# Kernel tuning notes

Hardware: AMD Instinct MI355X
Metric: run time of the kernel (lower is better)

The kernel has to match this reference:

```python
import jax, jax.numpy as jnp
import numpy as np

N = 50000      # nodes
E = 800000     # edges (avg degree 16)
D = 128        # hidden dim (hidden_dim = [128,128,128])
G = 500        # graphs in batch
NS = 100       # num_stock
M0 = 64        # mid_dim[0] == mid_dim[1]
M2 = 1         # mid_dim[2]
LRELU_SLOPE = 0.2
BN_EPS = 1e-5


def setup_inputs() -> dict:
    key = jax.random.key(0)
    ks = jax.random.split(key, 24)
    s = 0.05
    inp = {
        "x": jax.random.normal(ks[0], (N, D), dtype=jnp.float32),
        "graph_data": jax.random.randint(ks[1], (2, E), 0, N, dtype=jnp.int64)
            if jax.config.read("jax_enable_x64") else jax.random.randint(ks[1], (2, E), 0, N).astype(jnp.int32),
        "batch": jnp.sort(jax.random.randint(ks[2], (N,), 0, G)).astype(jnp.int32),
        # GATv2Conv layer 0 (in=D, out=D, heads=1)
        "wl0": jax.random.normal(ks[3], (D, D)) * s,
        "bl0": jax.random.normal(ks[4], (D,)) * s,
        "wr0": jax.random.normal(ks[5], (D, D)) * s,
        "br0": jax.random.normal(ks[6], (D,)) * s,
        "att0": jax.random.normal(ks[7], (D,)) * s,
        "b0": jax.random.normal(ks[8], (D,)) * s,
        # GATv2Conv layer 1
        "wl1": jax.random.normal(ks[9], (D, D)) * s,
        "bl1": jax.random.normal(ks[10], (D,)) * s,
        "wr1": jax.random.normal(ks[11], (D, D)) * s,
        "br1": jax.random.normal(ks[12], (D,)) * s,
        "att1": jax.random.normal(ks[13], (D,)) * s,
        "b1": jax.random.normal(ks[14], (D,)) * s,
        # BatchNorm1d (eval mode, running stats) applied after layer 0 only
        "bn_gamma": jnp.ones((D,), jnp.float32),
        "bn_beta": jnp.zeros((D,), jnp.float32),
        "bn_mean": jax.random.normal(ks[15], (D,)) * 0.1,
        "bn_var": jax.random.uniform(ks[16], (D,), minval=0.5, maxval=1.5),
        # fc1: hidden_dim[-2] -> num_stock*mid_dim[0]; fc3: mid_dim[1] -> mid_dim[2]
        "fc1_w": jax.random.normal(ks[17], (D, NS * M0)) * s,
        "fc1_b": jax.random.normal(ks[18], (NS * M0,)) * s,
        "fc3_w": jax.random.normal(ks[19], (M0, M2)) * s,
        "fc3_b": jax.random.normal(ks[20], (M2,)) * s,
    }
    return inp


def _gatv2(x, src, dst, wl, bl, wr, br, att, b):
    """PyG GATv2Conv, heads=1, add_self_loops=False, eval mode (no dropout)."""
    xl = x @ wl + bl                      # source-side transform [N, D]
    xr = x @ wr + br                      # target-side transform [N, D]
    # per-edge attention logits: a^T LeakyReLU(x_j + x_i)
    e = jnp.einsum("ed,d->e", jax.nn.leaky_relu(xl[src] + xr[dst], LRELU_SLOPE), att)
    # softmax over incoming edges of each destination node
    m = jax.ops.segment_max(e, dst, num_segments=N)
    m = jnp.where(jnp.isfinite(m), m, 0.0)
    p = jnp.exp(e - m[dst])
    denom = jax.ops.segment_sum(p, dst, num_segments=N)
    alpha = p / denom[dst]
    out = jax.ops.segment_sum(alpha[:, None] * xl[src], dst, num_segments=N)
    return out + b


def reference(x, graph_data, batch, wl0, bl0, wr0, br0, att0, b0,
              wl1, bl1, wr1, br1, att1, b1,
              bn_gamma, bn_beta, bn_mean, bn_var,
              fc1_w, fc1_b, fc3_w, fc3_b):
    src, dst = graph_data[0], graph_data[1]
    # layer 0: GATv2 -> BatchNorm (eval) -> ReLU
    h = _gatv2(x, src, dst, wl0, bl0, wr0, br0, att0, b0)
    h = bn_gamma * (h - bn_mean) * jax.lax.rsqrt(bn_var + BN_EPS) + bn_beta
    h = jax.nn.relu(h)
    # layer 1 (last): GATv2 only
    h = _gatv2(h, src, dst, wl1, bl1, wr1, br1, att1, b1)
    # global mean pool over graphs
    counts = jax.ops.segment_sum(jnp.ones((N,), h.dtype), batch, num_segments=G)
    pooled = jax.ops.segment_sum(h, batch, num_segments=G) / jnp.maximum(counts, 1.0)[:, None]
    # fc1 + reshape to [G, num_stock, mid_dim0]; dropout is eval-mode identity
    h = jax.nn.relu(pooled @ fc1_w + fc1_b).reshape(G, NS, M0)
    out = jax.nn.sigmoid(h @ fc3_w + fc3_b)   # [G, NS, 1]
    return out.reshape(G, NS * M2)
```

## Files before the change

### kernel.cpp

```cpp
#include <hip/hip_runtime.h>

#define DD 128
#define GG 500
#define NSTK 100
#define SLOPE 0.2f
#define BN_EPS 1e-5f
#define XPAD 136
#define SLOT 64

typedef __attribute__((ext_vector_type(8))) short bf16x8;
typedef __attribute__((ext_vector_type(4))) float f32x4;
typedef __attribute__((ext_vector_type(2))) float f32x2;
typedef unsigned int uint;
typedef unsigned short ushort;

static __device__ __forceinline__ ushort f2bf(float f) {
    union { float f; unsigned int u; } v; v.f = f;
    unsigned int r = (v.u + 0x7fff + ((v.u >> 16) & 1)) >> 16;
    return (ushort)r;
}

static __device__ __forceinline__ f32x2 bfpair(uint u) {
    union { uint2 u2; f32x2 f; } c;
    c.u2.x = u << 16;
    c.u2.y = u & 0xffff0000u;
    return c.f;
}


__global__ __launch_bounds__(128) void wprep_kernel(
    const float* __restrict__ wl0, const float* __restrict__ wr0,
    const float* __restrict__ wl1, const float* __restrict__ wr1,
    ushort* __restrict__ wt0, ushort* __restrict__ wt1,
    const float* __restrict__ bn_g, const float* __restrict__ bn_b,
    const float* __restrict__ bn_m, const float* __restrict__ bn_v,
    float* __restrict__ bn_scale, float* __restrict__ bn_shift)
{
    int c = blockIdx.x;
    int layer = blockIdx.y;
    int k = threadIdx.x;
    const float* wl = layer ? wl1 : wl0;
    const float* wr = layer ? wr1 : wr0;
    float v = (c < 128) ? wl[k * DD + c] : wr[k * DD + (c - 128)];
    (layer ? wt1 : wt0)[c * DD + k] = f2bf(v);
    if (c == 0 && layer == 0) {
        float s = bn_g[k] * rsqrtf(bn_v[k] + BN_EPS);
        bn_scale[k] = s;
        bn_shift[k] = bn_b[k] - bn_m[k] * s;
    }
}


__global__ __launch_bounds__(256) void mm0_scat_kernel(
    const int* __restrict__ src, const int* __restrict__ dst,
    int* __restrict__ deg, ushort* __restrict__ csr, int e_count, int MB,
    const float* __restrict__ x, const ushort* __restrict__ wt,
    const float* __restrict__ bA, const float* __restrict__ bB,
    ushort* __restrict__ outA, ushort* __restrict__ outB, int n)
{
    if ((int)blockIdx.x >= MB) {
        int e = ((int)blockIdx.x - MB) * 256 + threadIdx.x;
        if (e < e_count) {
            int d = dst[e];
            int r = atomicAdd(&deg[d], 1);
            if (r < SLOT) csr[d * SLOT + r] = (ushort)src[e];
        }
        return;
    }
    __shared__ ushort xs[32 * XPAD];
    int t = threadIdx.x;
    int row0 = (int)blockIdx.x * 32;

    #pragma unroll
    for (int i = 0; i < 2; ++i) {
        int idx8 = i * 256 + t;
        int r = idx8 >> 4;
        int c = (idx8 & 15) * 8;
        float4 v0 = make_float4(0.f, 0.f, 0.f, 0.f), v1 = v0;
        if (row0 + r < n) {
            v0 = *(const float4*)&x[(size_t)(row0 + r) * DD + c];
            v1 = *(const float4*)&x[(size_t)(row0 + r) * DD + c + 4];
        }
        union { bf16x8 v; ushort u[8]; } pk;
        pk.u[0] = f2bf(v0.x); pk.u[1] = f2bf(v0.y); pk.u[2] = f2bf(v0.z); pk.u[3] = f2bf(v0.w);
        pk.u[4] = f2bf(v1.x); pk.u[5] = f2bf(v1.y); pk.u[6] = f2bf(v1.z); pk.u[7] = f2bf(v1.w);
        *(bf16x8*)&xs[r * XPAD + c] = pk.v;
    }
    __syncthreads();

    int wave = t >> 6, lane = t & 63;
    int m16 = lane & 15;
    int kg = lane >> 4;

    bf16x8 bfr[4][4];
    #pragma unroll
    for (int ct = 0; ct < 4; ++ct) {
        int c = wave * 64 + ct * 16 + m16;
        #pragma unroll
        for (int ks = 0; ks < 4; ++ks)
            bfr[ks][ct] = *(const bf16x8*)&wt[(size_t)c * DD + ks * 32 + kg * 8];
    }

    f32x4 acc[2][4];
    #pragma unroll
    for (int rt = 0; rt < 2; ++rt)
        #pragma unroll
        for (int ct = 0; ct < 4; ++ct) acc[rt][ct] = (f32x4){0.f, 0.f, 0.f, 0.f};

    #pragma unroll
    for (int ks = 0; ks < 4; ++ks) {
        int koff = ks * 32 + kg * 8;
        bf16x8 a[2];
        #pragma unroll
        for (int rt = 0; rt < 2; ++rt)
            a[rt] = *(bf16x8*)&xs[(rt * 16 + m16) * XPAD + koff];
        #pragma unroll
        for (int rt = 0; rt < 2; ++rt)
            #pragma unroll
            for (int ct = 0; ct < 4; ++ct)
                acc[rt][ct] = __builtin_amdgcn_mfma_f32_16x16x32_bf16(a[rt], bfr[ks][ct], acc[rt][ct], 0, 0, 0);
    }

    #pragma unroll
    for (int rt = 0; rt < 2; ++rt) {
        int r0 = row0 + rt * 16 + kg * 4;
        #pragma unroll
        for (int ct = 0; ct < 4; ++ct) {
            int c = wave * 64 + ct * 16 + m16;
            float bb; ushort* op; int cc;
            if (c < 128) { bb = bA[c]; op = outA; cc = c; }
            else         { bb = bB[c - 128]; op = outB; cc = c - 128; }
            #pragma unroll
            for (int i = 0; i < 4; ++i) {
                if (r0 + i < n)
                    op[(size_t)(r0 + i) * DD + cc] = f2bf(acc[rt][ct][i] + bb);
            }
        }
    }
}


__global__ __launch_bounds__(256) void gat_agg_kernel(
    const ushort* __restrict__ xl, const ushort* __restrict__ xr,
    const int* __restrict__ degv, const ushort* __restrict__ csr,
    const float* __restrict__ att, const float* __restrict__ bias,
    const float* __restrict__ bn_scale, const float* __restrict__ bn_shift,
    ushort* __restrict__ out_bf, float* __restrict__ out_f32,
    int n, int use_bn)
{
    int wave = (int)((blockIdx.x * 256 + threadIdx.x) >> 6);
    int lane = threadIdx.x & 63;
    if (wave >= n) return;
    int grp = lane >> 4;
    int gl  = lane & 15;
    int f   = gl * 8;

    int deg = degv[wave];
    if (deg > SLOT) deg = SLOT;
    int sv = (lane < deg) ? (int)csr[(size_t)wave * SLOT + lane] : 0;

    uint4 xru = *(const uint4*)&xr[(size_t)wave * DD + f];
    f32x2 xrp[4] = {bfpair(xru.x), bfpair(xru.y), bfpair(xru.z), bfpair(xru.w)};
    const f32x2* attp = (const f32x2*)&att[f];
    f32x2 atp[4] = {attp[0], attp[1], attp[2], attp[3]};

    f32x2 accp[4] = {{0.f,0.f},{0.f,0.f},{0.f,0.f},{0.f,0.f}};
    float den = 0.f;

    int j0 = grp;
    uint4 a0 = make_uint4(0,0,0,0), a1 = make_uint4(0,0,0,0);
    if (j0 < deg) {
        int s = __shfl(sv, j0, 64);
        a0 = *(const uint4*)&xl[(size_t)s * DD + f];
    }
    if (j0 + 4 < deg) {
        int s = __shfl(sv, j0 + 4, 64);
        a1 = *(const uint4*)&xl[(size_t)s * DD + f];
    }

    for (int j = j0; j < deg; j += 4) {
        uint4 a2 = make_uint4(0,0,0,0);
        if (j + 8 < deg) {
            int s = __shfl(sv, j + 8, 64);
            a2 = *(const uint4*)&xl[(size_t)s * DD + f];
        }

        f32x2 ap[4] = {bfpair(a0.x), bfpair(a0.y), bfpair(a0.z), bfpair(a0.w)};
        f32x2 ld = {0.f, 0.f};
        #pragma unroll
        for (int k = 0; k < 4; ++k) {
            f32x2 tv = ap[k] + xrp[k];
            f32x2 lr = __builtin_elementwise_max(tv, SLOPE * tv);
            ld += atp[k] * lr;
        }
        float partial = ld.x + ld.y;
        partial += __shfl_xor(partial, 1, 64);
        partial += __shfl_xor(partial, 2, 64);
        partial += __shfl_xor(partial, 4, 64);
        partial += __shfl_xor(partial, 8, 64);
        float p = __expf(partial);
        den += p;
        #pragma unroll
        for (int k = 0; k < 4; ++k) accp[k] += p * ap[k];

        a0 = a1;
        a1 = a2;
    }

    float* accf = (float*)accp;
    #pragma unroll
    for (int k = 0; k < 8; ++k) {
        accf[k] += __shfl_xor(accf[k], 16, 64);
        accf[k] += __shfl_xor(accf[k], 32, 64);
    }
    den += __shfl_xor(den, 16, 64);
    den += __shfl_xor(den, 32, 64);

    if (grp == 0) {
        float inv = (deg > 0) ? 1.0f / den : 0.0f;
        float o[8];
        #pragma unroll
        for (int k = 0; k < 8; ++k) o[k] = accf[k] * inv + bias[f + k];
        if (use_bn) {
            #pragma unroll
            for (int k = 0; k < 8; ++k) {
                o[k] = o[k] * bn_scale[f + k] + bn_shift[f + k];
                o[k] = o[k] > 0.f ? o[k] : 0.f;
            }
        }
        if (out_bf) {
            uint4 pk;
            pk.x = ((uint)f2bf(o[1]) << 16) | f2bf(o[0]);
            pk.y = ((uint)f2bf(o[3]) << 16) | f2bf(o[2]);
            pk.z = ((uint)f2bf(o[5]) << 16) | f2bf(o[4]);
            pk.w = ((uint)f2bf(o[7]) << 16) | f2bf(o[6]);
            *(uint4*)&out_bf[(size_t)wave * DD + f] = pk;
        } else {
            *(float4*)&out_f32[(size_t)wave * DD + f]     = make_float4(o[0], o[1], o[2], o[3]);
            *(float4*)&out_f32[(size_t)wave * DD + f + 4] = make_float4(o[4], o[5], o[6], o[7]);
        }
    }
}


__global__ __launch_bounds__(256) void dualmm_mfma_kernel(
    const ushort* __restrict__ xbf,
    const ushort* __restrict__ wt,
    const float* __restrict__ bA, const float* __restrict__ bB,
    ushort* __restrict__ outA, ushort* __restrict__ outB, int n)
{
    __shared__ ushort xs[64 * XPAD];
    __shared__ ushort wsh[128 * XPAD];
    int t = threadIdx.x;
    int row0 = blockIdx.x * 64;

    #pragma unroll
    for (int i = 0; i < 4; ++i) {
        int idx = i * 256 + t;
        int r = idx >> 4;
        int c = (idx & 15) * 8;
        uint4 v = make_uint4(0, 0, 0, 0);
        if (row0 + r < n) v = *(const uint4*)&xbf[(size_t)(row0 + r) * DD + c];
        *(uint4*)&xs[r * XPAD + c] = v;
    }

    int wave = t >> 6, lane = t & 63;
    int m16 = lane & 15;
    int kg = lane >> 4;

    for (int half = 0; half < 2; ++half) {
        __syncthreads();
        #pragma unroll
        for (int i = 0; i < 8; ++i) {
            int idx = i * 256 + t;
            int r = idx >> 4;
            int ck = (idx & 15) * 8;
            uint4 v = *(const uint4*)&wt[(size_t)(half * 128 + r) * DD + ck];
            *(uint4*)&wsh[r * XPAD + ck] = v;
        }
        __syncthreads();

        f32x4 acc[4][2];
        #pragma unroll
        for (int rt = 0; rt < 4; ++rt)
            #pragma unroll
            for (int ct = 0; ct < 2; ++ct)
                acc[rt][ct] = (f32x4){0.f, 0.f, 0.f, 0.f};

        #pragma unroll
        for (int ks = 0; ks < 4; ++ks) {
            int koff = ks * 32 + kg * 8;
            bf16x8 a[4], b[2];
            #pragma unroll
            for (int rt = 0; rt < 4; ++rt)
                a[rt] = *(bf16x8*)&xs[(rt * 16 + m16) * XPAD + koff];
            #pragma unroll
            for (int ct = 0; ct < 2; ++ct)
                b[ct] = *(bf16x8*)&wsh[(wave * 32 + ct * 16 + m16) * XPAD + koff];
            #pragma unroll
            for (int rt = 0; rt < 4; ++rt)
                #pragma unroll
                for (int ct = 0; ct < 2; ++ct)
                    acc[rt][ct] = __builtin_amdgcn_mfma_f32_16x16x32_bf16(a[rt], b[ct], acc[rt][ct], 0, 0, 0);
        }

        const float* bias = half ? bB : bA;
        ushort* outp = half ? outB : outA;
        #pragma unroll
        for (int rt = 0; rt < 4; ++rt) {
            int r = row0 + rt * 16 + kg * 4;
            #pragma unroll
            for (int ct = 0; ct < 2; ++ct) {
                int c = wave * 32 + ct * 16 + m16;
                float bb = bias[c];
                #pragma unroll
                for (int i = 0; i < 4; ++i) {
                    if (r + i < n)
                        outp[(size_t)(r + i) * DD + c] = f2bf(acc[rt][ct][i] + bb);
                }
            }
        }
    }
}


__device__ __forceinline__ int lower_bound_dev(const int* __restrict__ arr, int n, int val) {
    int lo = 0, hi = n;
    while (lo < hi) {
        int mid = (lo + hi) >> 1;
        if (arr[mid] < val) lo = mid + 1; else hi = mid;
    }
    return lo;
}

__global__ __launch_bounds__(512) void pool_kernel(const float* __restrict__ h,
                                                   const int* __restrict__ batch,
                                                   float* __restrict__ pooled, int n) {
    __shared__ float red[4][DD];
    int g = blockIdx.x;
    int f = threadIdx.x & 127;
    int rg = threadIdx.x >> 7;
    int lo = lower_bound_dev(batch, n, g);
    int hi = lower_bound_dev(batch, n, g + 1);
    float s = 0.f;
    for (int i = lo + rg; i < hi; i += 4) s += h[(size_t)i * DD + f];
    red[rg][f] = s;
    __syncthreads();
    if (rg == 0) {
        float tot = red[0][f] + red[1][f] + red[2][f] + red[3][f];
        float cnt = (float)(hi - lo);
        pooled[(size_t)g * DD + f] = tot / fmaxf(cnt, 1.0f);
    }
}


__global__ __launch_bounds__(64) void head_kernel(
    const float* __restrict__ pooled, const float* __restrict__ fc1_w,
    const float* __restrict__ fc1_b, const float* __restrict__ fc3_w,
    const float* __restrict__ fc3_b, float* __restrict__ out)
{
    int sIdx = blockIdx.x;
    int gbase = blockIdx.y * 20;
    int j = threadIdx.x;

    float wreg[DD];
    #pragma unroll
    for (int k = 0; k < DD; ++k)
        wreg[k] = fc1_w[(size_t)k * (NSTK * 64) + sIdx * 64 + j];
    float b1 = fc1_b[sIdx * 64 + j];
    float w3 = fc3_w[j];
    float b3 = fc3_b[0];

    for (int gi = 0; gi < 20; ++gi) {
        int g = gbase + gi;
        float acc = b1;
        #pragma unroll
        for (int k4 = 0; k4 < DD / 4; ++k4) {
            float4 pv = *(const float4*)&pooled[(size_t)g * DD + k4 * 4];
            acc += pv.x * wreg[k4 * 4 + 0];
            acc += pv.y * wreg[k4 * 4 + 1];
            acc += pv.z * wreg[k4 * 4 + 2];
            acc += pv.w * wreg[k4 * 4 + 3];
        }
        float r = acc > 0.f ? acc : 0.f;
        float v = r * w3;
        #pragma unroll
        for (int off = 32; off; off >>= 1) v += __shfl_xor(v, off, 64);
        if (j == 0) out[(size_t)g * NSTK + sIdx] = 1.0f / (1.0f + __expf(-(v + b3)));
    }
}


extern "C" void kernel_launch(void* const* d_in, const int* in_sizes, int n_in,
                              void* d_out, int out_size, void* d_ws, size_t ws_size,
                              hipStream_t stream) {
    const float* x        = (const float*)d_in[0];
    const int*   graph    = (const int*)d_in[1];
    const int*   batch    = (const int*)d_in[2];
    const float* wl0      = (const float*)d_in[3];
    const float* bl0      = (const float*)d_in[4];
    const float* wr0      = (const float*)d_in[5];
    const float* br0      = (const float*)d_in[6];
    const float* att0     = (const float*)d_in[7];
    const float* b0       = (const float*)d_in[8];
    const float* wl1      = (const float*)d_in[9];
    const float* bl1      = (const float*)d_in[10];
    const float* wr1      = (const float*)d_in[11];
    const float* br1      = (const float*)d_in[12];
    const float* att1     = (const float*)d_in[13];
    const float* b1       = (const float*)d_in[14];
    const float* bn_gamma = (const float*)d_in[15];
    const float* bn_beta  = (const float*)d_in[16];
    const float* bn_mean  = (const float*)d_in[17];
    const float* bn_var   = (const float*)d_in[18];
    const float* fc1_w    = (const float*)d_in[19];
    const float* fc1_b    = (const float*)d_in[20];
    const float* fc3_w    = (const float*)d_in[21];
    const float* fc3_b    = (const float*)d_in[22];
    float* out = (float*)d_out;

    int n       = in_sizes[0] / DD;
    int e_count = in_sizes[1] / 2;
    const int* srcv = graph;
    const int* dstv = graph + e_count;

    ushort* A   = (ushort*)d_ws;
    ushort* B   = A  + (size_t)n * DD;
    ushort* Cb  = B  + (size_t)n * DD;
    float* Cf        = (float*)(Cb + (size_t)n * DD);
    float* pooled    = Cf + (size_t)n * DD;
    float* bn_scale  = pooled + (size_t)GG * DD;
    float* bn_shift  = bn_scale + DD;
    int* deg  = (int*)(bn_shift + DD);
    ushort* csr = (ushort*)(deg + n);
    uintptr_t wp = ((uintptr_t)(csr + (size_t)n * SLOT) + 15) & ~(uintptr_t)15;
    ushort* wt0 = (ushort*)wp;
    ushort* wt1 = wt0 + 256 * DD;

    int HB   = (e_count + 255) / 256;
    int MB32 = (n + 31) / 32;

    hipMemsetAsync(deg, 0, (size_t)n * sizeof(int), stream);
    wprep_kernel<<<dim3(256, 2), 128, 0, stream>>>(wl0, wr0, wl1, wr1, wt0, wt1,
                                                   bn_gamma, bn_beta, bn_mean, bn_var,
                                                   bn_scale, bn_shift);
    mm0_scat_kernel<<<MB32 + HB, 256, 0, stream>>>(srcv, dstv, deg, csr, e_count, MB32,
                                                   x, wt0, bl0, br0, A, B, n);
    gat_agg_kernel<<<(n + 3) / 4, 256, 0, stream>>>(A, B, deg, csr, att0, b0,
                                                    bn_scale, bn_shift, Cb, nullptr, n, 1);
    dualmm_mfma_kernel<<<(n + 63) / 64, 256, 0, stream>>>(Cb, wt1, bl1, br1, A, B, n);
    gat_agg_kernel<<<(n + 3) / 4, 256, 0, stream>>>(A, B, deg, csr, att1, b1,
                                                    nullptr, nullptr, nullptr, Cf, n, 0);
    pool_kernel<<<GG, 512, 0, stream>>>(Cf, batch, pooled, n);
    head_kernel<<<dim3(NSTK, GG / 20), 64, 0, stream>>>(pooled, fc1_w, fc1_b, fc3_w, fc3_b, out);
}
```

Baseline: 357.9 us.

## Split GAT aggregation across two waves per node and fold memset into prep

The aggregation kernel now gives each node two wavefronts, each handling half the edges with stride 8. Their partial sums are combined through shared memory after a block barrier. Separately, the degree-array memset is folded into the weight-prep kernel, and the scatter blocks now handle two edges per thread with nontemporal CSR stores, ordered before the matmul blocks. The changes aim to raise memory-level parallelism for low-degree gathers and remove a launch. In exchange they double the waves per node and add a barrier and shared-memory combine.

```diff
diff --git a/kernel.cpp b/kernel.cpp
--- a/kernel.cpp
+++ b/kernel.cpp
@@ -28,48 +28,62 @@
 }
 
 
-__global__ __launch_bounds__(128) void wprep_kernel(
+__global__ __launch_bounds__(128) void prep_kernel(
     const float* __restrict__ wl0, const float* __restrict__ wr0,
     const float* __restrict__ wl1, const float* __restrict__ wr1,
     ushort* __restrict__ wt0, ushort* __restrict__ wt1,
     const float* __restrict__ bn_g, const float* __restrict__ bn_b,
     const float* __restrict__ bn_m, const float* __restrict__ bn_v,
-    float* __restrict__ bn_scale, float* __restrict__ bn_shift)
+    float* __restrict__ bn_scale, float* __restrict__ bn_shift,
+    int* __restrict__ deg, int n)
 {
-    int c = blockIdx.x;
-    int layer = blockIdx.y;
-    int k = threadIdx.x;
-    const float* wl = layer ? wl1 : wl0;
-    const float* wr = layer ? wr1 : wr0;
-    float v = (c < 128) ? wl[k * DD + c] : wr[k * DD + (c - 128)];
-    (layer ? wt1 : wt0)[c * DD + k] = f2bf(v);
-    if (c == 0 && layer == 0) {
-        float s = bn_g[k] * rsqrtf(bn_v[k] + BN_EPS);
-        bn_scale[k] = s;
-        bn_shift[k] = bn_b[k] - bn_m[k] * s;
-    }
-}
-
-
-__global__ __launch_bounds__(256) void mm0_scat_kernel(
+    int bx = blockIdx.x;
+    if (bx < 512) {
+        int layer = bx >> 8;
+        int c = bx & 255;
+        int k = threadIdx.x;
+        const float* wl = layer ? wl1 : wl0;
+        const float* wr = layer ? wr1 : wr0;
+        float v = (c < 128) ? wl[k * DD + c] : wr[k * DD + (c - 128)];
+        (layer ? wt1 : wt0)[c * DD + k] = f2bf(v);
+        if (bx == 0) {
+            float s = bn_g[k] * rsqrtf(bn_v[k] + BN_EPS);
+            bn_scale[k] = s;
+            bn_shift[k] = bn_b[k] - bn_m[k] * s;
+        }
+    } else {
+        int i = (bx - 512) * 128 + threadIdx.x;
+        if (i < n) deg[i] = 0;
+    }
+}
+
+
+__global__ __launch_bounds__(256) void scat_mm0_kernel(
     const int* __restrict__ src, const int* __restrict__ dst,
-    int* __restrict__ deg, ushort* __restrict__ csr, int e_count, int MB,
+    int* __restrict__ deg, ushort* __restrict__ csr, int e_count, int SB,
     const float* __restrict__ x, const ushort* __restrict__ wt,
     const float* __restrict__ bA, const float* __restrict__ bB,
     ushort* __restrict__ outA, ushort* __restrict__ outB, int n)
 {
-    if ((int)blockIdx.x >= MB) {
-        int e = ((int)blockIdx.x - MB) * 256 + threadIdx.x;
-        if (e < e_count) {
-            int d = dst[e];
-            int r = atomicAdd(&deg[d], 1);
-            if (r < SLOT) csr[d * SLOT + r] = (ushort)src[e];
+    if ((int)blockIdx.x < SB) {
+        int e0 = (int)blockIdx.x * 512 + threadIdx.x;
+        int e1 = e0 + 256;
+        int d0 = 0, d1 = 0, s0 = 0, s1 = 0;
+        if (e0 < e_count) { d0 = dst[e0]; s0 = src[e0]; }
+        if (e1 < e_count) { d1 = dst[e1]; s1 = src[e1]; }
+        if (e0 < e_count) {
+            int r = atomicAdd(&deg[d0], 1);
+            if (r < SLOT) __builtin_nontemporal_store((ushort)s0, &csr[d0 * SLOT + r]);
+        }
+        if (e1 < e_count) {
+            int r = atomicAdd(&deg[d1], 1);
+            if (r < SLOT) __builtin_nontemporal_store((ushort)s1, &csr[d1 * SLOT + r]);
         }
         return;
     }
     __shared__ ushort xs[32 * XPAD];
     int t = threadIdx.x;
-    int row0 = (int)blockIdx.x * 32;
+    int row0 = ((int)blockIdx.x - SB) * 32;
 
     #pragma unroll
     for (int i = 0; i < 2; ++i) {
@@ -148,75 +162,90 @@
     ushort* __restrict__ out_bf, float* __restrict__ out_f32,
     int n, int use_bn)
 {
-    int wave = (int)((blockIdx.x * 256 + threadIdx.x) >> 6);
-    int lane = threadIdx.x & 63;
-    if (wave >= n) return;
-    int grp = lane >> 4;
-    int gl  = lane & 15;
-    int f   = gl * 8;
-
-    int deg = degv[wave];
-    if (deg > SLOT) deg = SLOT;
-    int sv = (lane < deg) ? (int)csr[(size_t)wave * SLOT + lane] : 0;
-
-    uint4 xru = *(const uint4*)&xr[(size_t)wave * DD + f];
-    f32x2 xrp[4] = {bfpair(xru.x), bfpair(xru.y), bfpair(xru.z), bfpair(xru.w)};
-    const f32x2* attp = (const f32x2*)&att[f];
-    f32x2 atp[4] = {attp[0], attp[1], attp[2], attp[3]};
-
-    f32x2 accp[4] = {{0.f,0.f},{0.f,0.f},{0.f,0.f},{0.f,0.f}};
+    __shared__ float comb[2][16][10];
+    int t = threadIdx.x;
+    int wave = t >> 6;
+    int lane = t & 63;
+    int half = wave & 1;
+    int slot = wave >> 1;
+    int node = blockIdx.x * 2 + slot;
+    int gl = lane & 15;
+    int f = gl * 8;
+    int grp8 = half * 4 + (lane >> 4);
+
+    bool valid = node < n;
+    float accf[8] = {0.f,0.f,0.f,0.f,0.f,0.f,0.f,0.f};
     float den = 0.f;
-
-    int j0 = grp;
-    uint4 a0 = make_uint4(0,0,0,0), a1 = make_uint4(0,0,0,0);
-    if (j0 < deg) {
-        int s = __shfl(sv, j0, 64);
-        a0 = *(const uint4*)&xl[(size_t)s * DD + f];
-    }
-    if (j0 + 4 < deg) {
-        int s = __shfl(sv, j0 + 4, 64);
-        a1 = *(const uint4*)&xl[(size_t)s * DD + f];
-    }
-
-    for (int j = j0; j < deg; j += 4) {
-        uint4 a2 = make_uint4(0,0,0,0);
-        if (j + 8 < deg) {
-            int s = __shfl(sv, j + 8, 64);
-            a2 = *(const uint4*)&xl[(size_t)s * DD + f];
-        }
-
-        f32x2 ap[4] = {bfpair(a0.x), bfpair(a0.y), bfpair(a0.z), bfpair(a0.w)};
-        f32x2 ld = {0.f, 0.f};
-        #pragma unroll
-        for (int k = 0; k < 4; ++k) {
-            f32x2 tv = ap[k] + xrp[k];
-            f32x2 lr = __builtin_elementwise_max(tv, SLOPE * tv);
-            ld += atp[k] * lr;
-        }
-        float partial = ld.x + ld.y;
-        partial += __shfl_xor(partial, 1, 64);
-        partial += __shfl_xor(partial, 2, 64);
-        partial += __shfl_xor(partial, 4, 64);
-        partial += __shfl_xor(partial, 8, 64);
-        float p = __expf(partial);
-        den += p;
-        #pragma unroll
-        for (int k = 0; k < 4; ++k) accp[k] += p * ap[k];
-
-        a0 = a1;
-        a1 = a2;
-    }
-
-    float* accf = (float*)accp;
-    #pragma unroll
-    for (int k = 0; k < 8; ++k) {
-        accf[k] += __shfl_xor(accf[k], 16, 64);
-        accf[k] += __shfl_xor(accf[k], 32, 64);
-    }
-    den += __shfl_xor(den, 16, 64);
-    den += __shfl_xor(den, 32, 64);
-
-    if (grp == 0) {
+    int deg = 0;
+
+    if (valid) {
+        deg = degv[node];
+        if (deg > SLOT) deg = SLOT;
+        int sv = (lane < deg) ? (int)csr[(size_t)node * SLOT + lane] : 0;
+
+        uint4 xru = *(const uint4*)&xr[(size_t)node * DD + f];
+        f32x2 xrp[4] = {bfpair(xru.x), bfpair(xru.y), bfpair(xru.z), bfpair(xru.w)};
+        const f32x2* attp = (const f32x2*)&att[f];
+        f32x2 atp[4] = {attp[0], attp[1], attp[2], attp[3]};
+
+        f32x2 accp[4] = {{0.f,0.f},{0.f,0.f},{0.f,0.f},{0.f,0.f}};
+
+        int j = grp8;
+        uint4 a0 = make_uint4(0,0,0,0);
+        if (j < deg) {
+            int s = __shfl(sv, j, 64);
+            a0 = *(const uint4*)&xl[(size_t)s * DD + f];
+        }
+        while (j < deg) {
+            uint4 a1 = make_uint4(0,0,0,0);
+            if (j + 8 < deg) {
+                int s = __shfl(sv, j + 8, 64);
+                a1 = *(const uint4*)&xl[(size_t)s * DD + f];
+            }
+            f32x2 ap[4] = {bfpair(a0.x), bfpair(a0.y), bfpair(a0.z), bfpair(a0.w)};
+            f32x2 ld = {0.f, 0.f};
+            #pragma unroll
+            for (int k = 0; k < 4; ++k) {
+                f32x2 tv = ap[k] + xrp[k];
+                f32x2 lr = __builtin_elementwise_max(tv, SLOPE * tv);
+                ld += atp[k] * lr;
+            }
+            float partial = ld.x + ld.y;
+            partial += __shfl_xor(partial, 1, 64);
+            partial += __shfl_xor(partial, 2, 64);
+            partial += __shfl_xor(partial, 4, 64);
+            partial += __shfl_xor(partial, 8, 64);
+            float p = __expf(partial);
+            den += p;
+            #pragma unroll
+            for (int k = 0; k < 4; ++k) accp[k] += p * ap[k];
+            a0 = a1;
+            j += 8;
+        }
+
+        float* af = (float*)accp;
+        #pragma unroll
+        for (int k = 0; k < 8; ++k) {
+            af[k] += __shfl_xor(af[k], 16, 64);
+            af[k] += __shfl_xor(af[k], 32, 64);
+            accf[k] = af[k];
+        }
+        den += __shfl_xor(den, 16, 64);
+        den += __shfl_xor(den, 32, 64);
+
+        if (half == 1 && lane < 16) {
+            #pragma unroll
+            for (int k = 0; k < 8; ++k) comb[slot][gl][k] = accf[k];
+            comb[slot][gl][8] = den;
+        }
+    }
+    __syncthreads();
+
+    if (valid && half == 0 && lane < 16) {
+        #pragma unroll
+        for (int k = 0; k < 8; ++k) accf[k] += comb[slot][gl][k];
+        den += comb[slot][gl][8];
+
         float inv = (deg > 0) ? 1.0f / den : 0.0f;
         float o[8];
         #pragma unroll
@@ -234,10 +263,10 @@
             pk.y = ((uint)f2bf(o[3]) << 16) | f2bf(o[2]);
             pk.z = ((uint)f2bf(o[5]) << 16) | f2bf(o[4]);
             pk.w = ((uint)f2bf(o[7]) << 16) | f2bf(o[6]);
-            *(uint4*)&out_bf[(size_t)wave * DD + f] = pk;
+            *(uint4*)&out_bf[(size_t)node * DD + f] = pk;
         } else {
-            *(float4*)&out_f32[(size_t)wave * DD + f]     = make_float4(o[0], o[1], o[2], o[3]);
-            *(float4*)&out_f32[(size_t)wave * DD + f + 4] = make_float4(o[4], o[5], o[6], o[7]);
+            *(float4*)&out_f32[(size_t)node * DD + f]     = make_float4(o[0], o[1], o[2], o[3]);
+            *(float4*)&out_f32[(size_t)node * DD + f + 4] = make_float4(o[4], o[5], o[6], o[7]);
         }
     }
 }
@@ -437,19 +466,19 @@
     ushort* wt0 = (ushort*)wp;
     ushort* wt1 = wt0 + 256 * DD;
 
-    int HB   = (e_count + 255) / 256;
+    int SB   = (e_count + 511) / 512;
     int MB32 = (n + 31) / 32;
-
-    hipMemsetAsync(deg, 0, (size_t)n * sizeof(int), stream);
-    wprep_kernel<<<dim3(256, 2), 128, 0, stream>>>(wl0, wr0, wl1, wr1, wt0, wt1,
-                                                   bn_gamma, bn_beta, bn_mean, bn_var,
-                                                   bn_scale, bn_shift);
-    mm0_scat_kernel<<<MB32 + HB, 256, 0, stream>>>(srcv, dstv, deg, csr, e_count, MB32,
+    int PB   = 512 + (n + 127) / 128;
+
+    prep_kernel<<<PB, 128, 0, stream>>>(wl0, wr0, wl1, wr1, wt0, wt1,
+                                        bn_gamma, bn_beta, bn_mean, bn_var,
+                                        bn_scale, bn_shift, deg, n);
+    scat_mm0_kernel<<<SB + MB32, 256, 0, stream>>>(srcv, dstv, deg, csr, e_count, SB,
                                                    x, wt0, bl0, br0, A, B, n);
-    gat_agg_kernel<<<(n + 3) / 4, 256, 0, stream>>>(A, B, deg, csr, att0, b0,
+    gat_agg_kernel<<<(n + 1) / 2, 256, 0, stream>>>(A, B, deg, csr, att0, b0,
                                                     bn_scale, bn_shift, Cb, nullptr, n, 1);
     dualmm_mfma_kernel<<<(n + 63) / 64, 256, 0, stream>>>(Cb, wt1, bl1, br1, A, B, n);
-    gat_agg_kernel<<<(n + 3) / 4, 256, 0, stream>>>(A, B, deg, csr, att1, b1,
+    gat_agg_kernel<<<(n + 1) / 2, 256, 0, stream>>>(A, B, deg, csr, att1, b1,
                                                     nullptr, nullptr, nullptr, Cf, n, 0);
     pool_kernel<<<GG, 512, 0, stream>>>(Cf, batch, pooled, n);
     head_kernel<<<dim3(NSTK, GG / 20), 64, 0, stream>>>(pooled, fc1_w, fc1_b, fc3_w, fc3_b, out);
```

Result: slower. 381.7 us (+6.7%).

## Fuse all stages into one persistent cooperative kernel with grid syncs

Applied to the files above, without the earlier changes.

Replaces the memset, weight prep, layer-0 matmul+scatter, two aggregation kernels, layer-1 matmul and pooling with a single persistent cooperative kernel. The stages run in grid-stride loops separated by grid.sync(). The layer-1 matmul now reuses the 32-row mm_unit path and drops the shared-memory weight-tiled dualmm kernel. The aim is to cut launch overhead and inter-kernel gaps, at the cost of grid-wide barriers, fewer resident blocks (occupancy-capped grid) and a changed matmul tiling.

```diff
diff --git a/kernel.cpp b/kernel.cpp
--- a/kernel.cpp
+++ b/kernel.cpp
@@ -1,4 +1,7 @@
 #include <hip/hip_runtime.h>
+#include <hip/hip_cooperative_groups.h>
+
+namespace cg = cooperative_groups;
 
 #define DD 128
 #define GG 500
@@ -28,63 +31,42 @@
 }
 
 
-__global__ __launch_bounds__(128) void wprep_kernel(
-    const float* __restrict__ wl0, const float* __restrict__ wr0,
-    const float* __restrict__ wl1, const float* __restrict__ wr1,
-    ushort* __restrict__ wt0, ushort* __restrict__ wt1,
-    const float* __restrict__ bn_g, const float* __restrict__ bn_b,
-    const float* __restrict__ bn_m, const float* __restrict__ bn_v,
-    float* __restrict__ bn_scale, float* __restrict__ bn_shift)
+static __device__ void mm_unit(int u, const float* __restrict__ xf,
+                               const ushort* __restrict__ xbf,
+                               const ushort* __restrict__ wt,
+                               const float* __restrict__ bA, const float* __restrict__ bB,
+                               ushort* __restrict__ outA, ushort* __restrict__ outB,
+                               int n, ushort* xs)
 {
-    int c = blockIdx.x;
-    int layer = blockIdx.y;
-    int k = threadIdx.x;
-    const float* wl = layer ? wl1 : wl0;
-    const float* wr = layer ? wr1 : wr0;
-    float v = (c < 128) ? wl[k * DD + c] : wr[k * DD + (c - 128)];
-    (layer ? wt1 : wt0)[c * DD + k] = f2bf(v);
-    if (c == 0 && layer == 0) {
-        float s = bn_g[k] * rsqrtf(bn_v[k] + BN_EPS);
-        bn_scale[k] = s;
-        bn_shift[k] = bn_b[k] - bn_m[k] * s;
-    }
-}
-
-
-__global__ __launch_bounds__(256) void mm0_scat_kernel(
-    const int* __restrict__ src, const int* __restrict__ dst,
-    int* __restrict__ deg, ushort* __restrict__ csr, int e_count, int MB,
-    const float* __restrict__ x, const ushort* __restrict__ wt,
-    const float* __restrict__ bA, const float* __restrict__ bB,
-    ushort* __restrict__ outA, ushort* __restrict__ outB, int n)
-{
-    if ((int)blockIdx.x >= MB) {
-        int e = ((int)blockIdx.x - MB) * 256 + threadIdx.x;
-        if (e < e_count) {
-            int d = dst[e];
-            int r = atomicAdd(&deg[d], 1);
-            if (r < SLOT) csr[d * SLOT + r] = (ushort)src[e];
-        }
-        return;
-    }
-    __shared__ ushort xs[32 * XPAD];
     int t = threadIdx.x;
-    int row0 = (int)blockIdx.x * 32;
-
-    #pragma unroll
-    for (int i = 0; i < 2; ++i) {
-        int idx8 = i * 256 + t;
-        int r = idx8 >> 4;
-        int c = (idx8 & 15) * 8;
-        float4 v0 = make_float4(0.f, 0.f, 0.f, 0.f), v1 = v0;
-        if (row0 + r < n) {
-            v0 = *(const float4*)&x[(size_t)(row0 + r) * DD + c];
-            v1 = *(const float4*)&x[(size_t)(row0 + r) * DD + c + 4];
-        }
-        union { bf16x8 v; ushort u[8]; } pk;
-        pk.u[0] = f2bf(v0.x); pk.u[1] = f2bf(v0.y); pk.u[2] = f2bf(v0.z); pk.u[3] = f2bf(v0.w);
-        pk.u[4] = f2bf(v1.x); pk.u[5] = f2bf(v1.y); pk.u[6] = f2bf(v1.z); pk.u[7] = f2bf(v1.w);
-        *(bf16x8*)&xs[r * XPAD + c] = pk.v;
+    int row0 = u * 32;
+
+    if (xf) {
+        #pragma unroll
+        for (int i = 0; i < 2; ++i) {
+            int idx8 = i * 256 + t;
+            int r = idx8 >> 4;
+            int c = (idx8 & 15) * 8;
+            float4 v0 = make_float4(0.f, 0.f, 0.f, 0.f), v1 = v0;
+            if (row0 + r < n) {
+                v0 = *(const float4*)&xf[(size_t)(row0 + r) * DD + c];
+                v1 = *(const float4*)&xf[(size_t)(row0 + r) * DD + c + 4];
+            }
+            union { bf16x8 v; ushort u[8]; } pk;
+            pk.u[0] = f2bf(v0.x); pk.u[1] = f2bf(v0.y); pk.u[2] = f2bf(v0.z); pk.u[3] = f2bf(v0.w);
+            pk.u[4] = f2bf(v1.x); pk.u[5] = f2bf(v1.y); pk.u[6] = f2bf(v1.z); pk.u[7] = f2bf(v1.w);
+            *(bf16x8*)&xs[r * XPAD + c] = pk.v;
+        }
+    } else {
+        #pragma unroll
+        for (int i = 0; i < 2; ++i) {
+            int idx8 = i * 256 + t;
+            int r = idx8 >> 4;
+            int c = (idx8 & 15) * 8;
+            uint4 v = make_uint4(0, 0, 0, 0);
+            if (row0 + r < n) v = *(const uint4*)&xbf[(size_t)(row0 + r) * DD + c];
+            *(uint4*)&xs[r * XPAD + c] = v;
+        }
     }
     __syncthreads();
 
@@ -137,29 +119,29 @@
             }
         }
     }
-}
-
-
-__global__ __launch_bounds__(256) void gat_agg_kernel(
-    const ushort* __restrict__ xl, const ushort* __restrict__ xr,
-    const int* __restrict__ degv, const ushort* __restrict__ csr,
-    const float* __restrict__ att, const float* __restrict__ bias,
-    const float* __restrict__ bn_scale, const float* __restrict__ bn_shift,
-    ushort* __restrict__ out_bf, float* __restrict__ out_f32,
-    int n, int use_bn)
+    __syncthreads();
+}
+
+
+static __device__ void agg_unit(int node, const ushort* __restrict__ xl,
+                                const ushort* __restrict__ xr,
+                                const int* __restrict__ degv, const ushort* __restrict__ csr,
+                                const float* __restrict__ att, const float* __restrict__ bias,
+                                const float* __restrict__ bn_scale, const float* __restrict__ bn_shift,
+                                ushort* __restrict__ out_bf, float* __restrict__ out_f32,
+                                int n, int use_bn)
 {
-    int wave = (int)((blockIdx.x * 256 + threadIdx.x) >> 6);
+    if (node >= n) return;
     int lane = threadIdx.x & 63;
-    if (wave >= n) return;
     int grp = lane >> 4;
     int gl  = lane & 15;
     int f   = gl * 8;
 
-    int deg = degv[wave];
+    int deg = degv[node];
     if (deg > SLOT) deg = SLOT;
-    int sv = (lane < deg) ? (int)csr[(size_t)wave * SLOT + lane] : 0;
-
-    uint4 xru = *(const uint4*)&xr[(size_t)wave * DD + f];
+    int sv = (lane < deg) ? (int)csr[(size_t)node * SLOT + lane] : 0;
+
+    uint4 xru = *(const uint4*)&xr[(size_t)node * DD + f];
     f32x2 xrp[4] = {bfpair(xru.x), bfpair(xru.y), bfpair(xru.z), bfpair(xru.w)};
     const f32x2* attp = (const f32x2*)&att[f];
     f32x2 atp[4] = {attp[0], attp[1], attp[2], attp[3]};
@@ -234,95 +216,13 @@
             pk.y = ((uint)f2bf(o[3]) << 16) | f2bf(o[2]);
             pk.z = ((uint)f2bf(o[5]) << 16) | f2bf(o[4]);
             pk.w = ((uint)f2bf(o[7]) << 16) | f2bf(o[6]);
-            *(uint4*)&out_bf[(size_t)wave * DD + f] = pk;
+            *(uint4*)&out_bf[(size_t)node * DD + f] = pk;
         } else {
-            *(float4*)&out_f32[(size_t)wave * DD + f]     = make_float4(o[0], o[1], o[2], o[3]);
-            *(float4*)&out_f32[(size_t)wave * DD + f + 4] = make_float4(o[4], o[5], o[6], o[7]);
-        }
-    }
-}
-
-
-__global__ __launch_bounds__(256) void dualmm_mfma_kernel(
-    const ushort* __restrict__ xbf,
-    const ushort* __restrict__ wt,
-    const float* __restrict__ bA, const float* __restrict__ bB,
-    ushort* __restrict__ outA, ushort* __restrict__ outB, int n)
-{
-    __shared__ ushort xs[64 * XPAD];
-    __shared__ ushort wsh[128 * XPAD];
-    int t = threadIdx.x;
-    int row0 = blockIdx.x * 64;
-
-    #pragma unroll
-    for (int i = 0; i < 4; ++i) {
-        int idx = i * 256 + t;
-        int r = idx >> 4;
-        int c = (idx & 15) * 8;
-        uint4 v = make_uint4(0, 0, 0, 0);
-        if (row0 + r < n) v = *(const uint4*)&xbf[(size_t)(row0 + r) * DD + c];
-        *(uint4*)&xs[r * XPAD + c] = v;
-    }
-
-    int wave = t >> 6, lane = t & 63;
-    int m16 = lane & 15;
-    int kg = lane >> 4;
-
-    for (int half = 0; half < 2; ++half) {
-        __syncthreads();
-        #pragma unroll
-        for (int i = 0; i < 8; ++i) {
-            int idx = i * 256 + t;
-            int r = idx >> 4;
-            int ck = (idx & 15) * 8;
-            uint4 v = *(const uint4*)&wt[(size_t)(half * 128 + r) * DD + ck];
-            *(uint4*)&wsh[r * XPAD + ck] = v;
-        }
-        __syncthreads();
-
-        f32x4 acc[4][2];
-        #pragma unroll
-        for (int rt = 0; rt < 4; ++rt)
-            #pragma unroll
-            for (int ct = 0; ct < 2; ++ct)
-                acc[rt][ct] = (f32x4){0.f, 0.f, 0.f, 0.f};
-
-        #pragma unroll
-        for (int ks = 0; ks < 4; ++ks) {
-            int koff = ks * 32 + kg * 8;
-            bf16x8 a[4], b[2];
-            #pragma unroll
-            for (int rt = 0; rt < 4; ++rt)
-                a[rt] = *(bf16x8*)&xs[(rt * 16 + m16) * XPAD + koff];
-            #pragma unroll
-            for (int ct = 0; ct < 2; ++ct)
-                b[ct] = *(bf16x8*)&wsh[(wave * 32 + ct * 16 + m16) * XPAD + koff];
-            #pragma unroll
-            for (int rt = 0; rt < 4; ++rt)
-                #pragma unroll
-                for (int ct = 0; ct < 2; ++ct)
-                    acc[rt][ct] = __builtin_amdgcn_mfma_f32_16x16x32_bf16(a[rt], b[ct], acc[rt][ct], 0, 0, 0);
-        }
-
-        const float* bias = half ? bB : bA;
-        ushort* outp = half ? outB : outA;
-        #pragma unroll
-        for (int rt = 0; rt < 4; ++rt) {
-            int r = row0 + rt * 16 + kg * 4;
-            #pragma unroll
-            for (int ct = 0; ct < 2; ++ct) {
-                int c = wave * 32 + ct * 16 + m16;
-                float bb = bias[c];
-                #pragma unroll
-                for (int i = 0; i < 4; ++i) {
-                    if (r + i < n)
-                        outp[(size_t)(r + i) * DD + c] = f2bf(acc[rt][ct][i] + bb);
-                }
-            }
-        }
-    }
-}
-
+            *(float4*)&out_f32[(size_t)node * DD + f]     = make_float4(o[0], o[1], o[2], o[3]);
+            *(float4*)&out_f32[(size_t)node * DD + f + 4] = make_float4(o[4], o[5], o[6], o[7]);
+        }
+    }
+}
 
 __device__ __forceinline__ int lower_bound_dev(const int* __restrict__ arr, int n, int val) {
     int lo = 0, hi = n;
@@ -333,23 +233,103 @@
     return lo;
 }
 
-__global__ __launch_bounds__(512) void pool_kernel(const float* __restrict__ h,
-                                                   const int* __restrict__ batch,
-                                                   float* __restrict__ pooled, int n) {
-    __shared__ float red[4][DD];
-    int g = blockIdx.x;
-    int f = threadIdx.x & 127;
-    int rg = threadIdx.x >> 7;
-    int lo = lower_bound_dev(batch, n, g);
-    int hi = lower_bound_dev(batch, n, g + 1);
-    float s = 0.f;
-    for (int i = lo + rg; i < hi; i += 4) s += h[(size_t)i * DD + f];
-    red[rg][f] = s;
-    __syncthreads();
-    if (rg == 0) {
-        float tot = red[0][f] + red[1][f] + red[2][f] + red[3][f];
-        float cnt = (float)(hi - lo);
-        pooled[(size_t)g * DD + f] = tot / fmaxf(cnt, 1.0f);
+
+__global__ __launch_bounds__(256, 6) void mega_kernel(
+    const float* __restrict__ x, const int* __restrict__ src, const int* __restrict__ dst,
+    const int* __restrict__ batch,
+    const float* __restrict__ wl0, const float* __restrict__ bl0,
+    const float* __restrict__ wr0, const float* __restrict__ br0,
+    const float* __restrict__ att0, const float* __restrict__ b0,
+    const float* __restrict__ wl1, const float* __restrict__ bl1,
+    const float* __restrict__ wr1, const float* __restrict__ br1,
+    const float* __restrict__ att1, const float* __restrict__ b1,
+    const float* __restrict__ bn_g, const float* __restrict__ bn_b,
+    const float* __restrict__ bn_m, const float* __restrict__ bn_v,
+    ushort* __restrict__ wt0, ushort* __restrict__ wt1,
+    float* __restrict__ bn_scale, float* __restrict__ bn_shift,
+    int* __restrict__ deg, ushort* __restrict__ csr,
+    ushort* __restrict__ A, ushort* __restrict__ B, ushort* __restrict__ Cb,
+    float* __restrict__ Cf, float* __restrict__ pooled,
+    int n, int e_count, int nblocks)
+{
+    __shared__ ushort xs[32 * XPAD];
+    cg::grid_group grid = cg::this_grid();
+    int b = blockIdx.x, t = threadIdx.x;
+
+    int degu = (n + 255) >> 8;
+    int prep_units = 257 + degu;
+    for (int u = b; u < prep_units; u += nblocks) {
+        if (u < 256) {
+            int idx = u * 256 + t;
+            int layer = idx >> 15;
+            int rem = idx & 32767;
+            int c = rem >> 7, k = rem & 127;
+            const float* wl = layer ? wl1 : wl0;
+            const float* wr = layer ? wr1 : wr0;
+            float v = (c < 128) ? wl[k * DD + c] : wr[k * DD + (c - 128)];
+            (layer ? wt1 : wt0)[c * DD + k] = f2bf(v);
+        } else if (u == 256) {
+            if (t < 128) {
+                float s = bn_g[t] * rsqrtf(bn_v[t] + BN_EPS);
+                bn_scale[t] = s;
+                bn_shift[t] = bn_b[t] - bn_m[t] * s;
+            }
+        } else {
+            int i = (u - 257) * 256 + t;
+            if (i < n) deg[i] = 0;
+        }
+    }
+    grid.sync();
+
+    int SB = (e_count + 255) >> 8;
+    int MB = (n + 31) >> 5;
+    for (int u = b; u < SB + MB; u += nblocks) {
+        if (u < SB) {
+            int e = u * 256 + t;
+            if (e < e_count) {
+                int d = dst[e];
+                int r = atomicAdd(&deg[d], 1);
+                if (r < SLOT) csr[d * SLOT + r] = (ushort)src[e];
+            }
+        } else {
+            mm_unit(u - SB, x, nullptr, wt0, bl0, br0, A, B, n, xs);
+        }
+    }
+    grid.sync();
+
+    int AGGU = (n + 3) >> 2;
+    for (int u = b; u < AGGU; u += nblocks) {
+        int node = u * 4 + (t >> 6);
+        agg_unit(node, A, B, deg, csr, att0, b0, bn_scale, bn_shift, Cb, nullptr, n, 1);
+    }
+    grid.sync();
+
+    for (int u = b; u < MB; u += nblocks)
+        mm_unit(u, nullptr, Cb, wt1, bl1, br1, A, B, n, xs);
+    grid.sync();
+
+    for (int u = b; u < AGGU; u += nblocks) {
+        int node = u * 4 + (t >> 6);
+        agg_unit(node, A, B, deg, csr, att1, b1, nullptr, nullptr, nullptr, Cf, n, 0);
+    }
+    grid.sync();
+
+    float* red = (float*)xs;
+    for (int g = b; g < GG; g += nblocks) {
+        int f = t & 127;
+        int rg = t >> 7;
+        int lo = lower_bound_dev(batch, n, g);
+        int hi = lower_bound_dev(batch, n, g + 1);
+        float s = 0.f;
+        for (int i = lo + rg; i < hi; i += 2) s += Cf[(size_t)i * DD + f];
+        red[rg * DD + f] = s;
+        __syncthreads();
+        if (rg == 0) {
+            float tot = red[f] + red[DD + f];
+            float cnt = (float)(hi - lo);
+            pooled[(size_t)g * DD + f] = tot / fmaxf(cnt, 1.0f);
+        }
+        __syncthreads();
     }
 }
 
@@ -437,20 +417,23 @@
     ushort* wt0 = (ushort*)wp;
     ushort* wt1 = wt0 + 256 * DD;
 
-    int HB   = (e_count + 255) / 256;
-    int MB32 = (n + 31) / 32;
-
-    hipMemsetAsync(deg, 0, (size_t)n * sizeof(int), stream);
-    wprep_kernel<<<dim3(256, 2), 128, 0, stream>>>(wl0, wr0, wl1, wr1, wt0, wt1,
-                                                   bn_gamma, bn_beta, bn_mean, bn_var,
-                                                   bn_scale, bn_shift);
-    mm0_scat_kernel<<<MB32 + HB, 256, 0, stream>>>(srcv, dstv, deg, csr, e_count, MB32,
-                                                   x, wt0, bl0, br0, A, B, n);
-    gat_agg_kernel<<<(n + 3) / 4, 256, 0, stream>>>(A, B, deg, csr, att0, b0,
-                                                    bn_scale, bn_shift, Cb, nullptr, n, 1);
-    dualmm_mfma_kernel<<<(n + 63) / 64, 256, 0, stream>>>(Cb, wt1, bl1, br1, A, B, n);
-    gat_agg_kernel<<<(n + 3) / 4, 256, 0, stream>>>(A, B, deg, csr, att1, b1,
-                                                    nullptr, nullptr, nullptr, Cf, n, 0);
-    pool_kernel<<<GG, 512, 0, stream>>>(Cf, batch, pooled, n);
+    int maxbpc = 0;
+    hipOccupancyMaxActiveBlocksPerMultiprocessor(&maxbpc, (const void*)mega_kernel, 256, 0);
+    if (maxbpc < 1) maxbpc = 1;
+    int nblocks = maxbpc * 256;
+    if (nblocks > 3328) nblocks = 3328;
+
+    void* kargs[] = {
+        (void*)&x, (void*)&srcv, (void*)&dstv, (void*)&batch,
+        (void*)&wl0, (void*)&bl0, (void*)&wr0, (void*)&br0, (void*)&att0, (void*)&b0,
+        (void*)&wl1, (void*)&bl1, (void*)&wr1, (void*)&br1, (void*)&att1, (void*)&b1,
+        (void*)&bn_gamma, (void*)&bn_beta, (void*)&bn_mean, (void*)&bn_var,
+        (void*)&wt0, (void*)&wt1, (void*)&bn_scale, (void*)&bn_shift,
+        (void*)&deg, (void*)&csr, (void*)&A, (void*)&B, (void*)&Cb,
+        (void*)&Cf, (void*)&pooled,
+        (void*)&n, (void*)&e_count, (void*)&nblocks
+    };
+    hipLaunchCooperativeKernel((void*)mega_kernel, dim3(nblocks), dim3(256),
+                               kargs, 0, stream);
     head_kernel<<<dim3(NSTK, GG / 20), 64, 0, stream>>>(pooled, fc1_w, fc1_b, fc3_w, fc3_b, out);
 }
```

Result: slower. 923.1 us (+157.9%).

## Fuse mean-pool into second GAT aggregation with atomics; merge prep and memset

Applied to the files above, without the earlier changes.

The second GAT aggregation now atomically accumulates each node's unnormalized output into the per-graph pooled sum instead of writing a full fp32 node matrix that a separate pool kernel reads back. The bias and the 1/count scaling move into the head kernel, with counts computed in a merged prep kernel that also zeros deg and pooled, replacing the memset and one launch. Edge-scatter blocks are also reordered to come before the matmul blocks. This removes an N×D fp32 write and read plus one kernel, at the cost of heavy float atomic contention on 500 graph rows and a nondeterministic summation order.

```diff
diff --git a/kernel.cpp b/kernel.cpp
--- a/kernel.cpp
+++ b/kernel.cpp
@@ -27,39 +27,68 @@
     return c.f;
 }
 
-
-__global__ __launch_bounds__(128) void wprep_kernel(
+__device__ __forceinline__ int lower_bound_dev(const int* __restrict__ arr, int n, int val) {
+    int lo = 0, hi = n;
+    while (lo < hi) {
+        int mid = (lo + hi) >> 1;
+        if (arr[mid] < val) lo = mid + 1; else hi = mid;
+    }
+    return lo;
+}
+
+
+__global__ __launch_bounds__(128) void prep_kernel(
     const float* __restrict__ wl0, const float* __restrict__ wr0,
     const float* __restrict__ wl1, const float* __restrict__ wr1,
     ushort* __restrict__ wt0, ushort* __restrict__ wt1,
     const float* __restrict__ bn_g, const float* __restrict__ bn_b,
     const float* __restrict__ bn_m, const float* __restrict__ bn_v,
-    float* __restrict__ bn_scale, float* __restrict__ bn_shift)
+    float* __restrict__ bn_scale, float* __restrict__ bn_shift,
+    int* __restrict__ deg, float* __restrict__ pooled,
+    const int* __restrict__ batch, float* __restrict__ inv_cnt,
+    int n, int DEGU)
 {
-    int c = blockIdx.x;
-    int layer = blockIdx.y;
-    int k = threadIdx.x;
-    const float* wl = layer ? wl1 : wl0;
-    const float* wr = layer ? wr1 : wr0;
-    float v = (c < 128) ? wl[k * DD + c] : wr[k * DD + (c - 128)];
-    (layer ? wt1 : wt0)[c * DD + k] = f2bf(v);
-    if (c == 0 && layer == 0) {
-        float s = bn_g[k] * rsqrtf(bn_v[k] + BN_EPS);
-        bn_scale[k] = s;
-        bn_shift[k] = bn_b[k] - bn_m[k] * s;
-    }
-}
-
-
-__global__ __launch_bounds__(256) void mm0_scat_kernel(
+    int bx = blockIdx.x;
+    int t = threadIdx.x;
+    if (bx < 512) {
+        int layer = bx >> 8;
+        int c = bx & 255;
+        const float* wl = layer ? wl1 : wl0;
+        const float* wr = layer ? wr1 : wr0;
+        float v = (c < 128) ? wl[t * DD + c] : wr[t * DD + (c - 128)];
+        (layer ? wt1 : wt0)[c * DD + t] = f2bf(v);
+        if (bx == 0) {
+            float s = bn_g[t] * rsqrtf(bn_v[t] + BN_EPS);
+            bn_scale[t] = s;
+            bn_shift[t] = bn_b[t] - bn_m[t] * s;
+        }
+    } else if (bx < 512 + DEGU) {
+        int i = (bx - 512) * 128 + t;
+        if (i < n) deg[i] = 0;
+    } else if (bx < 512 + DEGU + GG) {
+        int g = bx - 512 - DEGU;
+        pooled[(size_t)g * DD + t] = 0.f;
+    } else {
+        int g = (bx - 512 - DEGU - GG) * 128 + t;
+        if (g < GG) {
+            int lo = lower_bound_dev(batch, n, g);
+            int hi = lower_bound_dev(batch, n, g + 1);
+            float cnt = (float)(hi - lo);
+            inv_cnt[g] = 1.0f / fmaxf(cnt, 1.0f);
+        }
+    }
+}
+
+
+__global__ __launch_bounds__(256) void scat_mm0_kernel(
     const int* __restrict__ src, const int* __restrict__ dst,
-    int* __restrict__ deg, ushort* __restrict__ csr, int e_count, int MB,
+    int* __restrict__ deg, ushort* __restrict__ csr, int e_count, int SB,
     const float* __restrict__ x, const ushort* __restrict__ wt,
     const float* __restrict__ bA, const float* __restrict__ bB,
     ushort* __restrict__ outA, ushort* __restrict__ outB, int n)
 {
-    if ((int)blockIdx.x >= MB) {
-        int e = ((int)blockIdx.x - MB) * 256 + threadIdx.x;
+    if ((int)blockIdx.x < SB) {
+        int e = blockIdx.x * 256 + threadIdx.x;
         if (e < e_count) {
             int d = dst[e];
             int r = atomicAdd(&deg[d], 1);
@@ -69,7 +98,7 @@
     }
     __shared__ ushort xs[32 * XPAD];
     int t = threadIdx.x;
-    int row0 = (int)blockIdx.x * 32;
+    int row0 = ((int)blockIdx.x - SB) * 32;
 
     #pragma unroll
     for (int i = 0; i < 2; ++i) {
@@ -145,7 +174,8 @@
     const int* __restrict__ degv, const ushort* __restrict__ csr,
     const float* __restrict__ att, const float* __restrict__ bias,
     const float* __restrict__ bn_scale, const float* __restrict__ bn_shift,
-    ushort* __restrict__ out_bf, float* __restrict__ out_f32,
+    ushort* __restrict__ out_bf,
+    const int* __restrict__ batch, float* __restrict__ pooled,
     int n, int use_bn)
 {
     int wave = (int)((blockIdx.x * 256 + threadIdx.x) >> 6);
@@ -218,17 +248,17 @@
 
     if (grp == 0) {
         float inv = (deg > 0) ? 1.0f / den : 0.0f;
-        float o[8];
-        #pragma unroll
-        for (int k = 0; k < 8; ++k) o[k] = accf[k] * inv + bias[f + k];
-        if (use_bn) {
-            #pragma unroll
-            for (int k = 0; k < 8; ++k) {
-                o[k] = o[k] * bn_scale[f + k] + bn_shift[f + k];
-                o[k] = o[k] > 0.f ? o[k] : 0.f;
+        if (out_bf) {
+            float o[8];
+            #pragma unroll
+            for (int k = 0; k < 8; ++k) o[k] = accf[k] * inv + bias[f + k];
+            if (use_bn) {
+                #pragma unroll
+                for (int k = 0; k < 8; ++k) {
+                    o[k] = o[k] * bn_scale[f + k] + bn_shift[f + k];
+                    o[k] = o[k] > 0.f ? o[k] : 0.f;
+                }
             }
-        }
-        if (out_bf) {
             uint4 pk;
             pk.x = ((uint)f2bf(o[1]) << 16) | f2bf(o[0]);
             pk.y = ((uint)f2bf(o[3]) << 16) | f2bf(o[2]);
@@ -236,8 +266,10 @@
             pk.w = ((uint)f2bf(o[7]) << 16) | f2bf(o[6]);
             *(uint4*)&out_bf[(size_t)wave * DD + f] = pk;
         } else {
-            *(float4*)&out_f32[(size_t)wave * DD + f]     = make_float4(o[0], o[1], o[2], o[3]);
-            *(float4*)&out_f32[(size_t)wave * DD + f + 4] = make_float4(o[4], o[5], o[6], o[7]);
+            int g = batch[wave];
+            float* pr = &pooled[(size_t)g * DD + f];
+            #pragma unroll
+            for (int k = 0; k < 8; ++k) atomicAdd(&pr[k], accf[k] * inv);
         }
     }
 }
@@ -324,40 +356,12 @@
 }
 
 
-__device__ __forceinline__ int lower_bound_dev(const int* __restrict__ arr, int n, int val) {
-    int lo = 0, hi = n;
-    while (lo < hi) {
-        int mid = (lo + hi) >> 1;
-        if (arr[mid] < val) lo = mid + 1; else hi = mid;
-    }
-    return lo;
-}
-
-__global__ __launch_bounds__(512) void pool_kernel(const float* __restrict__ h,
-                                                   const int* __restrict__ batch,
-                                                   float* __restrict__ pooled, int n) {
-    __shared__ float red[4][DD];
-    int g = blockIdx.x;
-    int f = threadIdx.x & 127;
-    int rg = threadIdx.x >> 7;
-    int lo = lower_bound_dev(batch, n, g);
-    int hi = lower_bound_dev(batch, n, g + 1);
-    float s = 0.f;
-    for (int i = lo + rg; i < hi; i += 4) s += h[(size_t)i * DD + f];
-    red[rg][f] = s;
-    __syncthreads();
-    if (rg == 0) {
-        float tot = red[0][f] + red[1][f] + red[2][f] + red[3][f];
-        float cnt = (float)(hi - lo);
-        pooled[(size_t)g * DD + f] = tot / fmaxf(cnt, 1.0f);
-    }
-}
-
-
 __global__ __launch_bounds__(64) void head_kernel(
-    const float* __restrict__ pooled, const float* __restrict__ fc1_w,
-    const float* __restrict__ fc1_b, const float* __restrict__ fc3_w,
-    const float* __restrict__ fc3_b, float* __restrict__ out)
+    const float* __restrict__ pooled, const float* __restrict__ inv_cnt,
+    const float* __restrict__ gat_b,
+    const float* __restrict__ fc1_w, const float* __restrict__ fc1_b,
+    const float* __restrict__ fc3_w, const float* __restrict__ fc3_b,
+    float* __restrict__ out)
 {
     int sIdx = blockIdx.x;
     int gbase = blockIdx.y * 20;
@@ -373,14 +377,16 @@
 
     for (int gi = 0; gi < 20; ++gi) {
         int g = gbase + gi;
+        float invc = inv_cnt[g];
         float acc = b1;
         #pragma unroll
         for (int k4 = 0; k4 < DD / 4; ++k4) {
             float4 pv = *(const float4*)&pooled[(size_t)g * DD + k4 * 4];
-            acc += pv.x * wreg[k4 * 4 + 0];
-            acc += pv.y * wreg[k4 * 4 + 1];
-            acc += pv.z * wreg[k4 * 4 + 2];
-            acc += pv.w * wreg[k4 * 4 + 3];
+            float4 bv = *(const float4*)&gat_b[k4 * 4];
+            acc += (pv.x * invc + bv.x) * wreg[k4 * 4 + 0];
+            acc += (pv.y * invc + bv.y) * wreg[k4 * 4 + 1];
+            acc += (pv.z * invc + bv.z) * wreg[k4 * 4 + 2];
+            acc += (pv.w * invc + bv.w) * wreg[k4 * 4 + 3];
         }
         float r = acc > 0.f ? acc : 0.f;
         float v = r * w3;
@@ -427,30 +433,34 @@
     ushort* A   = (ushort*)d_ws;
     ushort* B   = A  + (size_t)n * DD;
     ushort* Cb  = B  + (size_t)n * DD;
-    float* Cf        = (float*)(Cb + (size_t)n * DD);
-    float* pooled    = Cf + (size_t)n * DD;
+    float* pooled    = (float*)(Cb + (size_t)n * DD);
     float* bn_scale  = pooled + (size_t)GG * DD;
     float* bn_shift  = bn_scale + DD;
-    int* deg  = (int*)(bn_shift + DD);
+    float* inv_cnt   = bn_shift + DD;
+    int* deg  = (int*)(inv_cnt + GG);
     ushort* csr = (ushort*)(deg + n);
     uintptr_t wp = ((uintptr_t)(csr + (size_t)n * SLOT) + 15) & ~(uintptr_t)15;
     ushort* wt0 = (ushort*)wp;
     ushort* wt1 = wt0 + 256 * DD;
 
-    int HB   = (e_count + 255) / 256;
+    int SB   = (e_count + 255) / 256;
     int MB32 = (n + 31) / 32;
-
-    hipMemsetAsync(deg, 0, (size_t)n * sizeof(int), stream);
-    wprep_kernel<<<dim3(256, 2), 128, 0, stream>>>(wl0, wr0, wl1, wr1, wt0, wt1,
-                                                   bn_gamma, bn_beta, bn_mean, bn_var,
-                                                   bn_scale, bn_shift);
-    mm0_scat_kernel<<<MB32 + HB, 256, 0, stream>>>(srcv, dstv, deg, csr, e_count, MB32,
+    int DEGU = (n + 127) / 128;
+    int PB   = 512 + DEGU + GG + (GG + 127) / 128;
+
+    prep_kernel<<<PB, 128, 0, stream>>>(wl0, wr0, wl1, wr1, wt0, wt1,
+                                        bn_gamma, bn_beta, bn_mean, bn_var,
+                                        bn_scale, bn_shift, deg, pooled,
+                                        batch, inv_cnt, n, DEGU);
+    scat_mm0_kernel<<<SB + MB32, 256, 0, stream>>>(srcv, dstv, deg, csr, e_count, SB,
                                                    x, wt0, bl0, br0, A, B, n);
     gat_agg_kernel<<<(n + 3) / 4, 256, 0, stream>>>(A, B, deg, csr, att0, b0,
-                                                    bn_scale, bn_shift, Cb, nullptr, n, 1);
+                                                    bn_scale, bn_shift, Cb,
+                                                    nullptr, nullptr, n, 1);
     dualmm_mfma_kernel<<<(n + 63) / 64, 256, 0, stream>>>(Cb, wt1, bl1, br1, A, B, n);
     gat_agg_kernel<<<(n + 3) / 4, 256, 0, stream>>>(A, B, deg, csr, att1, b1,
-                                                    nullptr, nullptr, nullptr, Cf, n, 0);
-    pool_kernel<<<GG, 512, 0, stream>>>(Cf, batch, pooled, n);
-    head_kernel<<<dim3(NSTK, GG / 20), 64, 0, stream>>>(pooled, fc1_w, fc1_b, fc3_w, fc3_b, out);
-}
+                                                    nullptr, nullptr, nullptr,
+                                                    batch, pooled, n, 0);
+    head_kernel<<<dim3(NSTK, GG / 20), 64, 0, stream>>>(pooled, inv_cnt, b1,
+                                                        fc1_w, fc1_b, fc3_w, fc3_b, out);
+}
```

New measurement: 569.9 us. 59.2% more time.
